# Kernel optimization log

Measured on AMD Instinct MI355X. Metric: run time of the kernel, lower is better.

## Reference

```python
import jax, jax.numpy as jnp
import numpy as np

N, D, OUT = 8192, 256, 256
NEG = -1e32  # matches torch softmax_with_mask


def setup_inputs() -> dict:
    key = jax.random.key(0)
    ks = jax.random.split(key, 5)
    features = jax.random.normal(ks[0], (N, D), dtype=jnp.float32)
    key_features = jax.random.normal(ks[1], (N, D), dtype=jnp.float32)
    adj_matrix = jax.random.uniform(ks[2], (N, N), dtype=jnp.float32)
    # Linear(2D -> OUT) and Linear(D -> OUT), torch layout W: [out, in]
    W_distill = jax.random.normal(ks[3], (OUT, 2 * D), dtype=jnp.float32) / np.sqrt(2 * D)
    b_distill = jnp.zeros((OUT,), dtype=jnp.float32)
    W_out = jax.random.normal(ks[4], (OUT, D), dtype=jnp.float32) / np.sqrt(D)
    b_out = jnp.zeros((OUT,), dtype=jnp.float32)
    return {"features": features, "key_features": key_features, "adj_matrix": adj_matrix,
            "W_distill": W_distill, "b_distill": b_distill, "W_out": W_out, "b_out": b_out}


def reference(features, key_features, adj_matrix, W_distill, b_distill, W_out, b_out):
    n = features.shape[0]
    # masked softmax over neighbors: mask out self-loop (diagonal)
    diag = jnp.eye(n, dtype=adj_matrix.dtype)
    logits = adj_matrix * 5.0 + diag * NEG  # (1 - mask) * -1e32
    w = jax.nn.softmax(logits, axis=-1)  # [N, N]
    # Original: sum_j w[i,j] * cat(f[i], f[j])  (never materialize [N,N,2D])
    head = features * jnp.sum(w, axis=-1, keepdims=True)  # [N, D]
    tail = w @ features                                    # [N, D]
    neigh_norm = jnp.concatenate([head, tail], axis=-1)    # [N, 2D]
    neigh = neigh_norm @ W_distill.T + b_distill           # [N, OUT]
    out = features @ W_out.T + b_out - neigh               # [N, OUT]
    out = jnp.tanh(out)  # activation=True; dropout is identity at eval
    return out
```

## Files before the change

kernel.cpp:

```cpp
#include <hip/hip_runtime.h>
#include <hip/hip_bf16.h>
#include <stdint.h>

#define N_NODES 8192
#define D_FEAT  256

typedef __bf16 bf16x8 __attribute__((ext_vector_type(8)));
typedef float  f32x4  __attribute__((ext_vector_type(4)));

__device__ __forceinline__ void async_copy16(const void* g, void* l) {
  __builtin_amdgcn_global_load_lds(
      (const __attribute__((address_space(1))) uint32_t*)g,
      (__attribute__((address_space(3))) uint32_t*)l,
      16, 0, 0);
}

__global__ void k_prep_ft(const float* __restrict__ F, __bf16* __restrict__ FT) {
  __shared__ float tile[32][33];
  int kb = blockIdx.x * 32;
  int nb = blockIdx.y * 32;
  int tx = threadIdx.x;
  int ty = threadIdx.y;
#pragma unroll
  for (int i = 0; i < 4; ++i) {
    int r = ty + i * 8;
    tile[r][tx] = F[(size_t)(kb + r) * 256 + nb + tx];
  }
  __syncthreads();
#pragma unroll
  for (int i = 0; i < 4; ++i) {
    int n = nb + ty + i * 8;
    int k = kb + tx;
    int e = k & 7, s = (k >> 3) & 7, base = k & ~63;
    int ks = base | ((s ^ (n & 7)) << 3) | e;
    FT[(size_t)n * 8192 + ks] = (__bf16)tile[tx][ty + i * 8];
  }
}

__global__ void k_prep_w(const float* __restrict__ Wd, const float* __restrict__ bd,
                         const float* __restrict__ Wo, const float* __restrict__ bo,
                         __bf16* __restrict__ W1, __bf16* __restrict__ W2,
                         float* __restrict__ cvec) {
  int o = blockIdx.x;
  int d = threadIdx.x;
  float w1 = Wo[(size_t)o * 256 + d] - Wd[(size_t)o * 512 + d];
  float w2 = -Wd[(size_t)o * 512 + 256 + d];
  W1[(size_t)o * 256 + d] = (__bf16)w1;
  W2[(size_t)o * 256 + d] = (__bf16)w2;
  if (d == 0) cvec[o] = bo[o] - bd[o];
}

__global__ __launch_bounds__(512, 4)
void k_main(const float* __restrict__ adj, const __bf16* __restrict__ FT,
            float* __restrict__ partial, float* __restrict__ pdenom,
            __bf16* __restrict__ tailbf,
            int kslog, int nk, int direct) {
  __shared__ __align__(16) char lds[81920];
  const int tid = threadIdx.x;
  const int bx = blockIdx.x;
  const int sp = bx & ((1 << kslog) - 1);
  const int mtile = bx >> kslog;
  const int r0 = mtile * 64;
  const int kbase = sp * (N_NODES >> kslog);

  const int rowl = tid >> 3;
  const int sl = tid & 7;
  const int rg = r0 + rowl;

  const float* ap = adj + (size_t)rg * N_NODES + kbase + sl * 8;

  float dsum = 0.f;

  f32x4 acc[2][4];
#pragma unroll
  for (int i = 0; i < 2; ++i)
#pragma unroll
    for (int j = 0; j < 4; ++j) acc[i][j] = (f32x4){0.f, 0.f, 0.f, 0.f};

  const int wv = tid >> 6;
  const int lane = tid & 63;
  const int wr = wv >> 2;
  const int wc = wv & 3;
  const int l15 = lane & 15;
  const int q = lane >> 4;

  const int awoff = rowl * 128 + ((sl ^ (rowl & 7)) << 4);

  auto issueB = [&](int ks, int bufsel) {
    const size_t kb2 = (size_t)(kbase + ks * 64) * 2;
    char* dst = lds + 16384 + bufsel * 32768;
#pragma unroll
    for (int i = 0; i < 4; ++i) {
      int off = (i * 512 + tid) * 16;
      const char* gsrc = (const char*)FT + (size_t)(off >> 7) * 16384 + kb2 + (off & 127);
      async_copy16(gsrc, dst + off);
    }
  };

  float4 c0 = *(const float4*)(ap);
  float4 c1 = *(const float4*)(ap + 4);
  __builtin_amdgcn_sched_barrier(0);
  issueB(0, 0);
  __builtin_amdgcn_sched_barrier(0);
  {
    float ev[8] = {c0.x, c0.y, c0.z, c0.w, c1.x, c1.y, c1.z, c1.w};
    const int kk = kbase + sl * 8;
    float s8 = 0.f;
    bf16x8 pk;
#pragma unroll
    for (int j = 0; j < 8; ++j) {
      float v = __expf(5.f * ev[j]);
      v = (kk + j == rg) ? 0.f : v;
      s8 += v;
      pk[j] = (__bf16)v;
    }
    dsum += s8;
    *(bf16x8*)(lds + awoff) = pk;
  }
  __builtin_amdgcn_sched_barrier(0);
  {
    int t = (1 < nk) ? 1 : 0;
    const float* apn = ap + (size_t)t * 64;
    c0 = *(const float4*)(apn);
    c1 = *(const float4*)(apn + 4);
  }
  __builtin_amdgcn_sched_barrier(0);

  for (int i = 0; i < nk; ++i) {
    const int cur = i & 1, nxt = cur ^ 1;
    asm volatile("s_waitcnt vmcnt(2) lgkmcnt(0)" ::: "memory");
    __builtin_amdgcn_sched_barrier(0);
    __builtin_amdgcn_s_barrier();
    __builtin_amdgcn_sched_barrier(0);

    issueB((i + 1 < nk) ? i + 1 : 0, nxt);
    __builtin_amdgcn_sched_barrier(0);

    {
      const char* bufAc = lds + cur * 8192;
      const char* bufBc = lds + 16384 + cur * 32768;
      __builtin_amdgcn_s_setprio(1);
#pragma unroll
      for (int kf = 0; kf < 2; ++kf) {
        const int slot = kf * 4 + q;
        bf16x8 af[2], bfr[4];
#pragma unroll
        for (int rf = 0; rf < 2; ++rf) {
          int row = wr * 32 + rf * 16 + l15;
          af[rf] = *(const bf16x8*)(bufAc + row * 128 + ((slot ^ (row & 7)) << 4));
        }
#pragma unroll
        for (int cf = 0; cf < 4; ++cf) {
          int nn = wc * 64 + cf * 16 + l15;
          bfr[cf] = *(const bf16x8*)(bufBc + nn * 128 + ((slot ^ (nn & 7)) << 4));
        }
#pragma unroll
        for (int rf = 0; rf < 2; ++rf)
#pragma unroll
          for (int cf = 0; cf < 4; ++cf)
            acc[rf][cf] = __builtin_amdgcn_mfma_f32_16x16x32_bf16(
                af[rf], bfr[cf], acc[rf][cf], 0, 0, 0);
      }
      __builtin_amdgcn_s_setprio(0);
    }
    if (i + 1 < nk) {
      float ev[8] = {c0.x, c0.y, c0.z, c0.w, c1.x, c1.y, c1.z, c1.w};
      const int kk = kbase + (i + 1) * 64 + sl * 8;
      float s8 = 0.f;
      bf16x8 pk;
#pragma unroll
      for (int j = 0; j < 8; ++j) {
        float v = __expf(5.f * ev[j]);
        v = (kk + j == rg) ? 0.f : v;
        s8 += v;
        pk[j] = (__bf16)v;
      }
      dsum += s8;
      *(bf16x8*)(lds + nxt * 8192 + awoff) = pk;
    }
    __builtin_amdgcn_sched_barrier(0);

    {
      int t = i + 2;
      if (t >= nk) t -= nk;
      const float* apn = ap + (size_t)t * 64;
      c0 = *(const float4*)(apn);
      c1 = *(const float4*)(apn + 4);
    }
    __builtin_amdgcn_sched_barrier(0);
  }

  asm volatile("s_waitcnt vmcnt(0)" ::: "memory");
  __builtin_amdgcn_sched_barrier(0);

  dsum += __shfl_xor(dsum, 1);
  dsum += __shfl_xor(dsum, 2);
  dsum += __shfl_xor(dsum, 4);

  if (direct) {
    float* dn = (float*)lds;
    __syncthreads();
    if (sl == 0) dn[rowl] = dsum;
    __syncthreads();
#pragma unroll
    for (int rf = 0; rf < 2; ++rf)
#pragma unroll
      for (int cf = 0; cf < 4; ++cf)
#pragma unroll
        for (int j = 0; j < 4; ++j) {
          int rl = wr * 32 + rf * 16 + q * 4 + j;
          int col = wc * 64 + cf * 16 + l15;
          tailbf[(size_t)(r0 + rl) * D_FEAT + col] = (__bf16)(acc[rf][cf][j] / dn[rl]);
        }
  } else {
    float* pout = partial + (size_t)sp * ((size_t)N_NODES * D_FEAT);
#pragma unroll
    for (int rf = 0; rf < 2; ++rf)
#pragma unroll
      for (int cf = 0; cf < 4; ++cf)
#pragma unroll
        for (int j = 0; j < 4; ++j) {
          int row = r0 + wr * 32 + rf * 16 + q * 4 + j;
          int col = wc * 64 + cf * 16 + l15;
          pout[(size_t)row * D_FEAT + col] = acc[rf][cf][j];
        }
    if (sl == 0) pdenom[(size_t)sp * N_NODES + rg] = dsum;
  }
}

__global__ void k_comb(const float* __restrict__ partial, const float* __restrict__ pden,
                       __bf16* __restrict__ tailbf, int ksplit) {
  int g = blockIdx.x * 256 + threadIdx.x;
  int row = g >> 6;
  int c4 = (g & 63) * 4;
  float4 v = {0.f, 0.f, 0.f, 0.f};
  float den = 0.f;
  for (int s = 0; s < ksplit; ++s) {
    const float* p = partial + (size_t)s * ((size_t)N_NODES * 256) + (size_t)row * 256 + c4;
    float4 u = *(const float4*)p;
    v.x += u.x; v.y += u.y; v.z += u.z; v.w += u.w;
    den += pden[(size_t)s * N_NODES + row];
  }
  float inv = 1.f / den;
  __bf16* o = tailbf + (size_t)row * 256 + c4;
  o[0] = (__bf16)(v.x * inv);
  o[1] = (__bf16)(v.y * inv);
  o[2] = (__bf16)(v.z * inv);
  o[3] = (__bf16)(v.w * inv);
}

__global__ __launch_bounds__(512)
void k_epi(const float* __restrict__ F, const __bf16* __restrict__ tailbf,
           const __bf16* __restrict__ W1, const __bf16* __restrict__ W2,
           const float* __restrict__ cvec, float* __restrict__ out) {
  const int tid = threadIdx.x;
  const int m0 = blockIdx.x * 32;
  const int wv = tid >> 6;
  const int lane = tid & 63;
  const int l15 = lane & 15;
  const int q = lane >> 4;
  const int col0 = wv * 32;

  f32x4 acc[2][2];
#pragma unroll
  for (int i = 0; i < 2; ++i)
#pragma unroll
    for (int j = 0; j < 2; ++j) acc[i][j] = (f32x4){0.f, 0.f, 0.f, 0.f};

#pragma unroll
  for (int kf = 0; kf < 8; ++kf) {
    bf16x8 a1[2], a2[2], b1[2], b2[2];
#pragma unroll
    for (int rf = 0; rf < 2; ++rf) {
      int row = m0 + rf * 16 + l15;
      const float* p = F + (size_t)row * 256 + kf * 32 + q * 8;
      float4 u0 = *(const float4*)p;
      float4 u1 = *(const float4*)(p + 4);
      float tmp[8] = {u0.x, u0.y, u0.z, u0.w, u1.x, u1.y, u1.z, u1.w};
#pragma unroll
      for (int j = 0; j < 8; ++j) a1[rf][j] = (__bf16)tmp[j];
      a2[rf] = *(const bf16x8*)(tailbf + (size_t)row * 256 + kf * 32 + q * 8);
    }
#pragma unroll
    for (int cf = 0; cf < 2; ++cf) {
      int col = col0 + cf * 16 + l15;
      b1[cf] = *(const bf16x8*)(W1 + (size_t)col * 256 + kf * 32 + q * 8);
      b2[cf] = *(const bf16x8*)(W2 + (size_t)col * 256 + kf * 32 + q * 8);
    }
#pragma unroll
    for (int rf = 0; rf < 2; ++rf)
#pragma unroll
      for (int cf = 0; cf < 2; ++cf) {
        acc[rf][cf] = __builtin_amdgcn_mfma_f32_16x16x32_bf16(a1[rf], b1[cf], acc[rf][cf], 0, 0, 0);
        acc[rf][cf] = __builtin_amdgcn_mfma_f32_16x16x32_bf16(a2[rf], b2[cf], acc[rf][cf], 0, 0, 0);
      }
  }
#pragma unroll
  for (int rf = 0; rf < 2; ++rf)
#pragma unroll
    for (int cf = 0; cf < 2; ++cf) {
      int col = col0 + cf * 16 + l15;
      float cb = cvec[col];
#pragma unroll
      for (int j = 0; j < 4; ++j) {
        int row = m0 + rf * 16 + q * 4 + j;
        out[(size_t)row * 256 + col] = tanhf(acc[rf][cf][j] + cb);
      }
    }
}

extern "C" void kernel_launch(void* const* d_in, const int* in_sizes, int n_in,
                              void* d_out, int out_size, void* d_ws, size_t ws_size,
                              hipStream_t stream) {
  (void)in_sizes; (void)n_in; (void)out_size;
  const float* features = (const float*)d_in[0];
  const float* adj = (const float*)d_in[2];
  const float* Wd  = (const float*)d_in[3];
  const float* bd  = (const float*)d_in[4];
  const float* Wo  = (const float*)d_in[5];
  const float* bo  = (const float*)d_in[6];
  float* out = (float*)d_out;

  char* ws = (char*)d_ws;
  const size_t SZ_FT   = (size_t)256 * 8192 * 2;
  const size_t SZ_W    = (size_t)256 * 256 * 2;
  const size_t SZ_C    = 256 * 4;
  const size_t SZ_TAIL = (size_t)8192 * 256 * 2;
  const size_t SZ_DEN  = (size_t)4 * 8192 * 4;
  const size_t SZ_P1   = (size_t)8192 * 256 * 4;

  const size_t offFT = 0;
  const size_t offW1 = offFT + SZ_FT;
  const size_t offW2 = offW1 + SZ_W;
  const size_t offC  = offW2 + SZ_W;
  const size_t offT  = offC + SZ_C;
  const size_t offD  = offT + SZ_TAIL;
  const size_t offP  = offD + SZ_DEN;

  int ksplit;
  if      (ws_size >= offP + 4 * SZ_P1) ksplit = 4;
  else if (ws_size >= offP + 2 * SZ_P1) ksplit = 2;
  else if (ws_size >= offP + 1 * SZ_P1) ksplit = 1;
  else                                  ksplit = 0;
  int direct = (ksplit == 0) ? 1 : 0;
  int kseff  = direct ? 1 : ksplit;
  int kslog  = (kseff == 4) ? 2 : (kseff == 2 ? 1 : 0);
  int nk     = (N_NODES / kseff) / 64;

  __bf16* FT     = (__bf16*)(ws + offFT);
  __bf16* W1     = (__bf16*)(ws + offW1);
  __bf16* W2     = (__bf16*)(ws + offW2);
  float*  cvec   = (float*)(ws + offC);
  __bf16* tailbf = (__bf16*)(ws + offT);
  float*  pden   = (float*)(ws + offD);
  float*  part   = (float*)(ws + offP);

  k_prep_ft<<<dim3(256, 8), dim3(32, 8), 0, stream>>>(features, FT);
  k_prep_w<<<256, 256, 0, stream>>>(Wd, bd, Wo, bo, W1, W2, cvec);
  k_main<<<128 * kseff, 512, 0, stream>>>(adj, FT, part, pden, tailbf, kslog, nk, direct);
  if (!direct)
    k_comb<<<2048, 256, 0, stream>>>(part, pden, tailbf, kseff);
  k_epi<<<256, 512, 0, stream>>>(features, tailbf, W1, W2, cvec, out);
}
```

Measured before the change: 434.7 us.

## Double k_main row tile to 128 and fuse split-K combine into epilogue

The main adjacency-times-features kernel now runs 1024-thread blocks covering 128 rows each, halving the block count. Each staged feature tile in LDS is therefore reused across twice as many rows, with a larger LDS footprint (96 KB) that lowers occupancy. The separate combine kernel is removed: the epilogue GEMM now sums the split-K partials and divides by the summed denominators while building its A operand. This saves a launch and the bf16 tail round trip through global memory, at the cost of more global reads inside the epilogue.

New measurement: 465.4 us. 7.1% more time.

```diff
diff --git a/kernel.cpp b/kernel.cpp
--- a/kernel.cpp
+++ b/kernel.cpp
@@ -50,17 +50,17 @@
   if (d == 0) cvec[o] = bo[o] - bd[o];
 }
 
-__global__ __launch_bounds__(512, 4)
+__global__ __launch_bounds__(1024, 4)
 void k_main(const float* __restrict__ adj, const __bf16* __restrict__ FT,
             float* __restrict__ partial, float* __restrict__ pdenom,
             __bf16* __restrict__ tailbf,
             int kslog, int nk, int direct) {
-  __shared__ __align__(16) char lds[81920];
+  __shared__ __align__(16) char lds[98304];
   const int tid = threadIdx.x;
   const int bx = blockIdx.x;
   const int sp = bx & ((1 << kslog) - 1);
   const int mtile = bx >> kslog;
-  const int r0 = mtile * 64;
+  const int r0 = mtile * 128;
   const int kbase = sp * (N_NODES >> kslog);
 
   const int rowl = tid >> 3;
@@ -88,10 +88,10 @@
 
   auto issueB = [&](int ks, int bufsel) {
     const size_t kb2 = (size_t)(kbase + ks * 64) * 2;
-    char* dst = lds + 16384 + bufsel * 32768;
-#pragma unroll
-    for (int i = 0; i < 4; ++i) {
-      int off = (i * 512 + tid) * 16;
+    char* dst = lds + 32768 + bufsel * 32768;
+#pragma unroll
+    for (int i = 0; i < 2; ++i) {
+      int off = (i * 1024 + tid) * 16;
       const char* gsrc = (const char*)FT + (size_t)(off >> 7) * 16384 + kb2 + (off & 127);
       async_copy16(gsrc, dst + off);
     }
@@ -137,8 +137,8 @@
     __builtin_amdgcn_sched_barrier(0);
 
     {
-      const char* bufAc = lds + cur * 8192;
-      const char* bufBc = lds + 16384 + cur * 32768;
+      const char* bufAc = lds + cur * 16384;
+      const char* bufBc = lds + 32768 + cur * 32768;
       __builtin_amdgcn_s_setprio(1);
 #pragma unroll
       for (int kf = 0; kf < 2; ++kf) {
@@ -176,7 +176,7 @@
         pk[j] = (__bf16)v;
       }
       dsum += s8;
-      *(bf16x8*)(lds + nxt * 8192 + awoff) = pk;
+      *(bf16x8*)(lds + nxt * 16384 + awoff) = pk;
     }
     __builtin_amdgcn_sched_barrier(0);
 
@@ -228,31 +228,13 @@
   }
 }
 
-__global__ void k_comb(const float* __restrict__ partial, const float* __restrict__ pden,
-                       __bf16* __restrict__ tailbf, int ksplit) {
-  int g = blockIdx.x * 256 + threadIdx.x;
-  int row = g >> 6;
-  int c4 = (g & 63) * 4;
-  float4 v = {0.f, 0.f, 0.f, 0.f};
-  float den = 0.f;
-  for (int s = 0; s < ksplit; ++s) {
-    const float* p = partial + (size_t)s * ((size_t)N_NODES * 256) + (size_t)row * 256 + c4;
-    float4 u = *(const float4*)p;
-    v.x += u.x; v.y += u.y; v.z += u.z; v.w += u.w;
-    den += pden[(size_t)s * N_NODES + row];
-  }
-  float inv = 1.f / den;
-  __bf16* o = tailbf + (size_t)row * 256 + c4;
-  o[0] = (__bf16)(v.x * inv);
-  o[1] = (__bf16)(v.y * inv);
-  o[2] = (__bf16)(v.z * inv);
-  o[3] = (__bf16)(v.w * inv);
-}
-
 __global__ __launch_bounds__(512)
-void k_epi(const float* __restrict__ F, const __bf16* __restrict__ tailbf,
+void k_epi(const float* __restrict__ F,
+           const float* __restrict__ partial, const float* __restrict__ pden,
+           const __bf16* __restrict__ tailbf,
            const __bf16* __restrict__ W1, const __bf16* __restrict__ W2,
-           const float* __restrict__ cvec, float* __restrict__ out) {
+           const float* __restrict__ cvec, float* __restrict__ out,
+           int ksplit, int direct) {
   const int tid = threadIdx.x;
   const int m0 = blockIdx.x * 32;
   const int wv = tid >> 6;
@@ -267,6 +249,18 @@
 #pragma unroll
     for (int j = 0; j < 2; ++j) acc[i][j] = (f32x4){0.f, 0.f, 0.f, 0.f};
 
+  float invden[2];
+#pragma unroll
+  for (int rf = 0; rf < 2; ++rf) {
+    int row = m0 + rf * 16 + l15;
+    if (direct) { invden[rf] = 1.f; }
+    else {
+      float den = 0.f;
+      for (int s = 0; s < ksplit; ++s) den += pden[(size_t)s * N_NODES + row];
+      invden[rf] = 1.f / den;
+    }
+  }
+
 #pragma unroll
   for (int kf = 0; kf < 8; ++kf) {
     bf16x8 a1[2], a2[2], b1[2], b2[2];
@@ -279,7 +273,21 @@
       float tmp[8] = {u0.x, u0.y, u0.z, u0.w, u1.x, u1.y, u1.z, u1.w};
 #pragma unroll
       for (int j = 0; j < 8; ++j) a1[rf][j] = (__bf16)tmp[j];
-      a2[rf] = *(const bf16x8*)(tailbf + (size_t)row * 256 + kf * 32 + q * 8);
+      if (direct) {
+        a2[rf] = *(const bf16x8*)(tailbf + (size_t)row * 256 + kf * 32 + q * 8);
+      } else {
+        float t8[8] = {0.f, 0.f, 0.f, 0.f, 0.f, 0.f, 0.f, 0.f};
+        for (int s = 0; s < ksplit; ++s) {
+          const float* pp = partial + (size_t)s * ((size_t)N_NODES * 256)
+                          + (size_t)row * 256 + kf * 32 + q * 8;
+          float4 v0 = *(const float4*)pp;
+          float4 v1 = *(const float4*)(pp + 4);
+          t8[0] += v0.x; t8[1] += v0.y; t8[2] += v0.z; t8[3] += v0.w;
+          t8[4] += v1.x; t8[5] += v1.y; t8[6] += v1.z; t8[7] += v1.w;
+        }
+#pragma unroll
+        for (int j = 0; j < 8; ++j) a2[rf][j] = (__bf16)(t8[j] * invden[rf]);
+      }
     }
 #pragma unroll
     for (int cf = 0; cf < 2; ++cf) {
@@ -357,8 +365,6 @@
 
   k_prep_ft<<<dim3(256, 8), dim3(32, 8), 0, stream>>>(features, FT);
   k_prep_w<<<256, 256, 0, stream>>>(Wd, bd, Wo, bo, W1, W2, cvec);
-  k_main<<<128 * kseff, 512, 0, stream>>>(adj, FT, part, pden, tailbf, kslog, nk, direct);
-  if (!direct)
-    k_comb<<<2048, 256, 0, stream>>>(part, pden, tailbf, kseff);
-  k_epi<<<256, 512, 0, stream>>>(features, tailbf, W1, W2, cvec, out);
-}
+  k_main<<<64 * kseff, 1024, 0, stream>>>(adj, FT, part, pden, tailbf, kslog, nk, direct);
+  k_epi<<<256, 512, 0, stream>>>(features, part, pden, tailbf, W1, W2, cvec, out, kseff, direct);
+}
```
